# Kernel tuning notes

Measured on AMD Instinct MI355X. Metric: run time of the kernel, lower is better.

## Reference

```python
import jax, jax.numpy as jnp
import numpy as np

DIM = 1024
N_HEADS = 16
HEAD_DIM = DIM // N_HEADS
SCALE = HEAD_DIM ** (-0.5)


def setup_inputs() -> dict:
    key = jax.random.key(0)
    ks = jax.random.split(key, 5)
    B, N = 2, 2048
    x = jax.random.normal(ks[0], (B, N, DIM), dtype=jnp.float32)
    # torch nn.Linear weight layout: (out_features, in_features)
    qkv_w = jax.random.normal(ks[1], (3 * DIM, DIM), dtype=jnp.float32) * 0.02
    qkv_b = jax.random.normal(ks[2], (3 * DIM,), dtype=jnp.float32) * 0.02
    proj_w = jax.random.normal(ks[3], (DIM, DIM), dtype=jnp.float32) * 0.02
    proj_b = jax.random.normal(ks[4], (DIM,), dtype=jnp.float32) * 0.02
    return {"x": x, "qkv_w": qkv_w, "qkv_b": qkv_b, "proj_w": proj_w, "proj_b": proj_b}


def reference(x, qkv_w, qkv_b, proj_w, proj_b):
    B, N, C = x.shape
    # QKV projection: (B,N,C) -> (B,N,3C)
    qkv = jnp.einsum('bnc,oc->bno', x, qkv_w) + qkv_b
    # (B,N,3,H,Dh) -> (3,B,H,N,Dh)
    qkv = qkv.reshape(B, N, 3, N_HEADS, HEAD_DIM).transpose(2, 0, 3, 1, 4)
    q, k, v = qkv[0], qkv[1], qkv[2]
    attn = jnp.einsum('bhqd,bhkd->bhqk', q, k) * SCALE
    attn = jax.nn.softmax(attn, axis=-1)
    out = jnp.einsum('bhqk,bhkd->bhqd', attn, v)
    out = out.transpose(0, 2, 1, 3).reshape(B, N, C)  # concat heads
    out = jnp.einsum('bnc,oc->bno', out, proj_w) + proj_b
    return out
```

## Files before the change

### kernel.cpp

```cpp
#include <hip/hip_runtime.h>

#define DIM 1024
#define NHEADS 16
#define HD 64
#define NSEQ 2048
#define MROWS 4096
#define QKV_LD 3072

typedef __attribute__((ext_vector_type(8))) short short8;
typedef __attribute__((ext_vector_type(4))) short short4v;
typedef __attribute__((ext_vector_type(4))) float f32x4;

typedef __attribute__((address_space(1))) void gvoid_t;
typedef __attribute__((address_space(3))) void lvoid_t;

#if __has_builtin(__builtin_amdgcn_exp2f)
#define EXP2(x) __builtin_amdgcn_exp2f(x)
#else
#define EXP2(x) exp2f(x)
#endif

#if __has_builtin(__builtin_amdgcn_mfma_f32_16x16x16_bf16)
#define MFMA16(a, b, c) __builtin_amdgcn_mfma_f32_16x16x16_bf16(a, b, c, 0, 0, 0)
#elif __has_builtin(__builtin_amdgcn_mfma_f32_16x16x16bf16_1k)
#define MFMA16(a, b, c) __builtin_amdgcn_mfma_f32_16x16x16bf16_1k(a, b, c, 0, 0, 0)
#else
static __device__ __forceinline__ f32x4 mfma16_asm(short4v a, short4v b, f32x4 c) {
  __asm__("v_mfma_f32_16x16x16_bf16 %0, %1, %2, %0" : "+v"(c) : "v"(a), "v"(b));
  return c;
}
#define MFMA16(a, b, c) mfma16_asm(a, b, c)
#endif

#define EXP_SCALE 0.18033688011112042f

__device__ __forceinline__ unsigned short f2bf(float f) {
  unsigned int u = __builtin_bit_cast(unsigned int, f);
  u += 0x7FFFu + ((u >> 16) & 1u);
  return (unsigned short)(u >> 16);
}

__device__ __forceinline__ void gl_lds16(const void* g, void* l) {
  __builtin_amdgcn_global_load_lds((gvoid_t*)g, (lvoid_t*)l, 16, 0, 0);
}

__global__ __launch_bounds__(256) void cast_bf16_3(
    const float* __restrict__ x, const float* __restrict__ wq,
    const float* __restrict__ wp,
    unsigned short* __restrict__ xb, unsigned short* __restrict__ wqb,
    unsigned short* __restrict__ wpb)
{
  int g = blockIdx.x * 256 + threadIdx.x;
  const float* src;
  unsigned short* dst;
  if (g < 1048576)            { src = x  + (size_t)g * 4;              dst = xb  + (size_t)g * 4; }
  else if (g < 1048576 + 786432) { int t = g - 1048576; src = wq + (size_t)t * 4; dst = wqb + (size_t)t * 4; }
  else                        { int t = g - 1048576 - 786432; src = wp + (size_t)t * 4; dst = wpb + (size_t)t * 4; }
  float4 v = *(const float4*)src;
  ushort4 o;
  o.x = f2bf(v.x); o.y = f2bf(v.y); o.z = f2bf(v.z); o.w = f2bf(v.w);
  *(ushort4*)dst = o;
}

__global__ __launch_bounds__(256) void gemm_nt(
    const unsigned short* __restrict__ A,
    const unsigned short* __restrict__ Bw,
    const float* __restrict__ bias,
    int K, int mode,
    unsigned short* __restrict__ oq,
    unsigned short* __restrict__ ovt,
    float* __restrict__ of)
{
  __shared__ unsigned short As[128 * 32];
  __shared__ unsigned short Bs[128 * 32];

  const int tid  = threadIdx.x;
  const int wave = tid >> 6, lane = tid & 63;
  const int quad = lane >> 4, l15 = lane & 15;
  const int mblk = blockIdx.x * 128;
  const int nblk = blockIdx.y * 128;
  const int wrow = (wave >> 1) * 64, wcol = (wave & 1) * 64;

  f32x4 acc[4][4] = {};

  const int sr = lane >> 2;
  const int sq = (lane & 3) ^ (sr & 3);
  const unsigned short* aBase = A  + (size_t)(mblk + wave * 32 + sr) * K + sq * 8;
  const unsigned short* bBase = Bw + (size_t)(nblk + wave * 32 + sr) * K + sq * 8;

  for (int k0 = 0; k0 < K; k0 += 32) {
    __syncthreads();
    gl_lds16(aBase + k0,          As + (wave * 32) * 32);
    gl_lds16(aBase + 16 * K + k0, As + (wave * 32 + 16) * 32);
    gl_lds16(bBase + k0,          Bs + (wave * 32) * 32);
    gl_lds16(bBase + 16 * K + k0, Bs + (wave * 32 + 16) * 32);
    __syncthreads();

    short8 af[4], bf8[4];
#pragma unroll
    for (int mt = 0; mt < 4; ++mt) {
      int row = wrow + mt * 16 + l15;
      af[mt] = *(const short8*)(As + row * 32 + ((quad ^ (row & 3)) * 8));
    }
#pragma unroll
    for (int nt = 0; nt < 4; ++nt) {
      int row = wcol + nt * 16 + l15;
      bf8[nt] = *(const short8*)(Bs + row * 32 + ((quad ^ (row & 3)) * 8));
    }
#pragma unroll
    for (int mt = 0; mt < 4; ++mt)
#pragma unroll
      for (int nt = 0; nt < 4; ++nt)
        acc[mt][nt] = __builtin_amdgcn_mfma_f32_16x16x32_bf16(af[mt], bf8[nt], acc[mt][nt], 0, 0, 0);
  }

  float bv[4];
#pragma unroll
  for (int nt = 0; nt < 4; ++nt) bv[nt] = bias[nblk + wcol + nt * 16 + l15];

  if (mode == 0) {
#pragma unroll
    for (int mt = 0; mt < 4; ++mt) {
      int row0 = mblk + wrow + mt * 16 + quad * 4;
#pragma unroll
      for (int nt = 0; nt < 4; ++nt) {
        int col = nblk + wcol + nt * 16 + l15;
#pragma unroll
        for (int r = 0; r < 4; ++r)
          of[(size_t)(row0 + r) * DIM + col] = acc[mt][nt][r] + bv[nt];
      }
    }
  } else if (nblk < 2048) {
    const float qs = (nblk < 1024) ? EXP_SCALE : 1.0f;
#pragma unroll
    for (int mt = 0; mt < 4; ++mt) {
      int row0 = mblk + wrow + mt * 16 + quad * 4;
#pragma unroll
      for (int nt = 0; nt < 4; ++nt) {
        int col = nblk + wcol + nt * 16 + l15;
#pragma unroll
        for (int r = 0; r < 4; ++r)
          oq[(size_t)(row0 + r) * QKV_LD + col] = f2bf((acc[mt][nt][r] + bv[nt]) * qs);
      }
    }
  } else {
#pragma unroll
    for (int mt = 0; mt < 4; ++mt) {
      int row0 = mblk + wrow + mt * 16 + quad * 4;
      int n0 = row0 & (NSEQ - 1);
      int bb = row0 >> 11;
#pragma unroll
      for (int nt = 0; nt < 4; ++nt) {
        int colr = (nblk - 2048) + wcol + nt * 16 + l15;
        int bh = bb * NHEADS + (colr >> 6);
        int d  = colr & 63;
        ushort4 pk;
        pk.x = f2bf(acc[mt][nt][0] + bv[nt]);
        pk.y = f2bf(acc[mt][nt][1] + bv[nt]);
        pk.z = f2bf(acc[mt][nt][2] + bv[nt]);
        pk.w = f2bf(acc[mt][nt][3] + bv[nt]);
        *(ushort4*)(ovt + ((size_t)bh * HD + d) * NSEQ + n0) = pk;
      }
    }
  }
}

__global__ __launch_bounds__(256) void gemm_nt64(
    const unsigned short* __restrict__ A,
    const unsigned short* __restrict__ Bw,
    const float* __restrict__ bias,
    int K,
    float* __restrict__ of)
{
  __shared__ unsigned short As[64 * 32];
  __shared__ unsigned short Bs[128 * 32];

  const int tid  = threadIdx.x;
  const int wave = tid >> 6, lane = tid & 63;
  const int quad = lane >> 4, l15 = lane & 15;
  const int mblk = blockIdx.x * 64;
  const int nblk = blockIdx.y * 128;
  const int wrow = (wave >> 1) * 32, wcol = (wave & 1) * 64;

  f32x4 acc[2][4] = {};

  const int sr = lane >> 2;
  const int sq = (lane & 3) ^ (sr & 3);
  const unsigned short* aBase = A  + (size_t)(mblk + wave * 16 + sr) * K + sq * 8;
  const unsigned short* bBase = Bw + (size_t)(nblk + wave * 32 + sr) * K + sq * 8;

  for (int k0 = 0; k0 < K; k0 += 32) {
    __syncthreads();
    gl_lds16(aBase + k0,          As + (wave * 16) * 32);
    gl_lds16(bBase + k0,          Bs + (wave * 32) * 32);
    gl_lds16(bBase + 16 * K + k0, Bs + (wave * 32 + 16) * 32);
    __syncthreads();

    short8 af[2], bf8[4];
#pragma unroll
    for (int mt = 0; mt < 2; ++mt) {
      int row = wrow + mt * 16 + l15;
      af[mt] = *(const short8*)(As + row * 32 + ((quad ^ (row & 3)) * 8));
    }
#pragma unroll
    for (int nt = 0; nt < 4; ++nt) {
      int row = wcol + nt * 16 + l15;
      bf8[nt] = *(const short8*)(Bs + row * 32 + ((quad ^ (row & 3)) * 8));
    }
#pragma unroll
    for (int mt = 0; mt < 2; ++mt)
#pragma unroll
      for (int nt = 0; nt < 4; ++nt)
        acc[mt][nt] = __builtin_amdgcn_mfma_f32_16x16x32_bf16(af[mt], bf8[nt], acc[mt][nt], 0, 0, 0);
  }

  float bv[4];
#pragma unroll
  for (int nt = 0; nt < 4; ++nt) bv[nt] = bias[nblk + wcol + nt * 16 + l15];

#pragma unroll
  for (int mt = 0; mt < 2; ++mt) {
    int row0 = mblk + wrow + mt * 16 + quad * 4;
#pragma unroll
    for (int nt = 0; nt < 4; ++nt) {
      int col = nblk + wcol + nt * 16 + l15;
#pragma unroll
      for (int r = 0; r < 4; ++r)
        of[(size_t)(row0 + r) * DIM + col] = acc[mt][nt][r] + bv[nt];
    }
  }
}

__global__ __launch_bounds__(256, 4) void attn_fused(
    const unsigned short* __restrict__ qkv,
    const unsigned short* __restrict__ vt,
    unsigned short* __restrict__ aout)
{
  __shared__ unsigned short Ks[64 * 64];
  __shared__ unsigned short Vs[64 * 64];

  const int tid  = threadIdx.x;
  const int wave = tid >> 6, lane = tid & 63;
  const int quad = lane >> 4, l15 = lane & 15;
  const int bh = blockIdx.x, b = bh >> 4, h = bh & 15;
  const int q0 = blockIdx.y * 64;
  const size_t qkvB = (size_t)b * NSEQ * QKV_LD;

  short8 qf[2];
#pragma unroll
  for (int ks = 0; ks < 2; ++ks)
    qf[ks] = *(const short8*)(qkv + qkvB +
        (size_t)(q0 + wave * 16 + l15) * QKV_LD + h * HD + ks * 32 + quad * 8);

  f32x4 oacc[4] = {};
  float lsum = 0.f;

  const int sr8 = lane >> 3;
  const int sp8 = lane & 7;

  const int r0s = wave * 16 + sr8;
  const int r1s = wave * 16 + 8 + sr8;
  const int qc0 = sp8 ^ (r0s & 7);
  const int qc1 = sp8 ^ (r1s & 7);
  const unsigned short* kBase = qkv + qkvB + DIM + h * HD;
  const unsigned short* vBase = vt + (size_t)bh * HD * NSEQ;
  const unsigned short* kSrc0 = kBase + (size_t)r0s * QKV_LD + qc0 * 8;
  const unsigned short* kSrc1 = kBase + (size_t)r1s * QKV_LD + qc1 * 8;
  const unsigned short* vSrc0 = vBase + (size_t)r0s * NSEQ + qc0 * 8;
  const unsigned short* vSrc1 = vBase + (size_t)r1s * NSEQ + qc1 * 8;

  for (int kk = 0; kk < NSEQ; kk += 64) {
    __syncthreads();
    gl_lds16(kSrc0 + (size_t)kk * QKV_LD, Ks + (wave * 16) * 64);
    gl_lds16(kSrc1 + (size_t)kk * QKV_LD, Ks + (wave * 16 + 8) * 64);
    gl_lds16(vSrc0 + kk,                  Vs + (wave * 16) * 64);
    gl_lds16(vSrc1 + kk,                  Vs + (wave * 16 + 8) * 64);
    __syncthreads();

    short8 kf[4][2];
#pragma unroll
    for (int kt = 0; kt < 4; ++kt)
#pragma unroll
      for (int ks = 0; ks < 2; ++ks) {
        int row = kt * 16 + l15;
        kf[kt][ks] = *(const short8*)(Ks + row * 64 + (((ks * 4 + quad) ^ (row & 7)) * 8));
      }

    f32x4 sacc[4] = {};
    __builtin_amdgcn_s_setprio(1);
#pragma unroll
    for (int kt = 0; kt < 4; ++kt) {
      sacc[kt] = __builtin_amdgcn_mfma_f32_16x16x32_bf16(kf[kt][0], qf[0], sacc[kt], 0, 0, 0);
      sacc[kt] = __builtin_amdgcn_mfma_f32_16x16x32_bf16(kf[kt][1], qf[1], sacc[kt], 0, 0, 0);
    }
    __builtin_amdgcn_s_setprio(0);

    short4v vf[4][4];
#pragma unroll
    for (int dt = 0; dt < 4; ++dt) {
      int row = dt * 16 + l15;
      int rw  = row & 7;
      const unsigned short* vb = Vs + row * 64 + (quad & 1) * 4;
#pragma unroll
      for (int kt = 0; kt < 4; ++kt) {
        int phys = (2 * kt + (quad >> 1)) ^ rw;
        vf[dt][kt] = *(const short4v*)(vb + phys * 8);
      }
    }

#pragma unroll
    for (int kt = 0; kt < 4; ++kt) {
      float p0 = EXP2(sacc[kt][0]);
      float p1 = EXP2(sacc[kt][1]);
      float p2 = EXP2(sacc[kt][2]);
      float p3 = EXP2(sacc[kt][3]);
      lsum += (p0 + p1) + (p2 + p3);
      unsigned r0 = __builtin_bit_cast(unsigned, p0) + 0x8000u;
      unsigned r1 = __builtin_bit_cast(unsigned, p1) + 0x8000u;
      unsigned r2 = __builtin_bit_cast(unsigned, p2) + 0x8000u;
      unsigned r3 = __builtin_bit_cast(unsigned, p3) + 0x8000u;
      uint2 pd;
      pd.x = __builtin_amdgcn_perm(r1, r0, 0x07060302u);
      pd.y = __builtin_amdgcn_perm(r3, r2, 0x07060302u);
      short4v pf = __builtin_bit_cast(short4v, pd);
      __builtin_amdgcn_s_setprio(1);
#pragma unroll
      for (int dt = 0; dt < 4; ++dt)
        oacc[dt] = MFMA16(vf[dt][kt], pf, oacc[dt]);
      __builtin_amdgcn_s_setprio(0);
    }
  }

  lsum += __shfl_xor(lsum, 16);
  lsum += __shfl_xor(lsum, 32);
  float inv = 1.0f / lsum;

  const int qrow = q0 + wave * 16 + l15;
  const size_t outBase = (size_t)(b * NSEQ + qrow) * DIM + h * HD;
#pragma unroll
  for (int dt = 0; dt < 4; ++dt) {
    unsigned a0 = __builtin_bit_cast(unsigned, oacc[dt][0] * inv) + 0x8000u;
    unsigned a1 = __builtin_bit_cast(unsigned, oacc[dt][1] * inv) + 0x8000u;
    unsigned a2 = __builtin_bit_cast(unsigned, oacc[dt][2] * inv) + 0x8000u;
    unsigned a3 = __builtin_bit_cast(unsigned, oacc[dt][3] * inv) + 0x8000u;
    uint2 st;
    st.x = __builtin_amdgcn_perm(a1, a0, 0x07060302u);
    st.y = __builtin_amdgcn_perm(a3, a2, 0x07060302u);
    *(uint2*)(aout + outBase + dt * 16 + quad * 4) = st;
  }
}

extern "C" void kernel_launch(void* const* d_in, const int* in_sizes, int n_in,
                              void* d_out, int out_size, void* d_ws, size_t ws_size,
                              hipStream_t stream) {
  (void)in_sizes; (void)n_in; (void)out_size; (void)ws_size;
  const float* x      = (const float*)d_in[0];
  const float* qkv_w  = (const float*)d_in[1];
  const float* qkv_b  = (const float*)d_in[2];
  const float* proj_w = (const float*)d_in[3];
  const float* proj_b = (const float*)d_in[4];
  float* out = (float*)d_out;

  char* ws = (char*)d_ws;
  unsigned short* xb   = (unsigned short*)(ws);
  unsigned short* wqb  = (unsigned short*)(ws + ( 8u << 20));
  unsigned short* wpb  = (unsigned short*)(ws + (14u << 20));
  unsigned short* qkv  = (unsigned short*)(ws + (16u << 20));
  unsigned short* vtw  = (unsigned short*)(ws + (40u << 20));
  unsigned short* attn = (unsigned short*)(ws + (48u << 20));

  cast_bf16_3<<<8192, 256, 0, stream>>>(x, qkv_w, proj_w, xb, wqb, wpb);
  gemm_nt<<<dim3(32, 24), 256, 0, stream>>>(xb, wqb, qkv_b, DIM, 1, qkv, vtw, nullptr);
  attn_fused<<<dim3(32, 32), 256, 0, stream>>>(qkv, vtw, attn);
  gemm_nt64<<<dim3(64, 8), 256, 0, stream>>>(attn, wpb, proj_b, DIM, out);
}
```

Measured before the change: 192.8 us.

## Double-buffer K/V tiles in attention and store V in MFMA fragment order

The QKV GEMM epilogue now writes V directly in a pre-swizzled fragment layout that matches the per-lane MFMA operand order. The attention kernel can then read V fragments with contiguous 16-byte LDS loads instead of several swizzled 8-byte loads. K/V LDS tiles are double-buffered so the global-to-LDS copy of the next tile overlaps compute on the current tile, leaving one barrier per iteration. LDS use doubles, which may reduce occupancy at 4 blocks per CU, and the V layout is now coupled between the two kernels.

```diff
diff --git a/kernel.cpp b/kernel.cpp
--- a/kernel.cpp
+++ b/kernel.cpp
@@ -149,17 +149,24 @@
       int row0 = mblk + wrow + mt * 16 + quad * 4;
       int n0 = row0 & (NSEQ - 1);
       int bb = row0 >> 11;
+      int tt  = n0 >> 6;
+      int kin = n0 & 63;
+      int kt  = kin >> 4;
+      int qv  = (kin >> 2) & 3;
 #pragma unroll
       for (int nt = 0; nt < 4; ++nt) {
         int colr = (nblk - 2048) + wcol + nt * 16 + l15;
         int bh = bb * NHEADS + (colr >> 6);
         int d  = colr & 63;
+        int dt = d >> 4, dl15 = d & 15;
         ushort4 pk;
         pk.x = f2bf(acc[mt][nt][0] + bv[nt]);
         pk.y = f2bf(acc[mt][nt][1] + bv[nt]);
         pk.z = f2bf(acc[mt][nt][2] + bv[nt]);
         pk.w = f2bf(acc[mt][nt][3] + bv[nt]);
-        *(ushort4*)(ovt + ((size_t)bh * HD + d) * NSEQ + n0) = pk;
+        size_t off = (size_t)(bh * 32 + tt) * 4096 + kt * 1024 + (dt >> 1) * 512
+                   + qv * 128 + dl15 * 8 + (dt & 1) * 4;
+        *(ushort4*)(ovt + off) = pk;
       }
     }
   }
@@ -233,11 +240,11 @@
 
 __global__ __launch_bounds__(256, 4) void attn_fused(
     const unsigned short* __restrict__ qkv,
-    const unsigned short* __restrict__ vt,
+    const unsigned short* __restrict__ vfrag,
     unsigned short* __restrict__ aout)
 {
-  __shared__ unsigned short Ks[64 * 64];
-  __shared__ unsigned short Vs[64 * 64];
+  __shared__ unsigned short Ks[2][64 * 64];
+  __shared__ unsigned short Vs[2][64 * 64];
 
   const int tid  = threadIdx.x;
   const int wave = tid >> 6, lane = tid & 63;
@@ -263,19 +270,28 @@
   const int qc0 = sp8 ^ (r0s & 7);
   const int qc1 = sp8 ^ (r1s & 7);
   const unsigned short* kBase = qkv + qkvB + DIM + h * HD;
-  const unsigned short* vBase = vt + (size_t)bh * HD * NSEQ;
   const unsigned short* kSrc0 = kBase + (size_t)r0s * QKV_LD + qc0 * 8;
   const unsigned short* kSrc1 = kBase + (size_t)r1s * QKV_LD + qc1 * 8;
-  const unsigned short* vSrc0 = vBase + (size_t)r0s * NSEQ + qc0 * 8;
-  const unsigned short* vSrc1 = vBase + (size_t)r1s * NSEQ + qc1 * 8;
+  const unsigned short* vfT = vfrag + (size_t)bh * 32 * 4096 + wave * 512 + lane * 8;
+
+  auto stage = [&](int bufi, int kkn) {
+    gl_lds16(kSrc0 + (size_t)kkn * QKV_LD, &Ks[bufi][(wave * 16) * 64]);
+    gl_lds16(kSrc1 + (size_t)kkn * QKV_LD, &Ks[bufi][(wave * 16 + 8) * 64]);
+    const unsigned short* vs = vfT + (size_t)(kkn >> 6) * 4096;
+    gl_lds16(vs,        &Vs[bufi][wave * 512]);
+    gl_lds16(vs + 2048, &Vs[bufi][wave * 512 + 2048]);
+  };
+
+  stage(0, 0);
+  asm volatile("s_waitcnt vmcnt(0)" ::: "memory");
+  __syncthreads();
 
   for (int kk = 0; kk < NSEQ; kk += 64) {
-    __syncthreads();
-    gl_lds16(kSrc0 + (size_t)kk * QKV_LD, Ks + (wave * 16) * 64);
-    gl_lds16(kSrc1 + (size_t)kk * QKV_LD, Ks + (wave * 16 + 8) * 64);
-    gl_lds16(vSrc0 + kk,                  Vs + (wave * 16) * 64);
-    gl_lds16(vSrc1 + kk,                  Vs + (wave * 16 + 8) * 64);
-    __syncthreads();
+    const int cur = (kk >> 6) & 1;
+    if (kk + 64 < NSEQ) stage(cur ^ 1, kk + 64);
+
+    const unsigned short* Kc = Ks[cur];
+    const unsigned short* Vc = Vs[cur];
 
     short8 kf[4][2];
 #pragma unroll
@@ -283,7 +299,7 @@
 #pragma unroll
       for (int ks = 0; ks < 2; ++ks) {
         int row = kt * 16 + l15;
-        kf[kt][ks] = *(const short8*)(Ks + row * 64 + (((ks * 4 + quad) ^ (row & 7)) * 8));
+        kf[kt][ks] = *(const short8*)(Kc + row * 64 + (((ks * 4 + quad) ^ (row & 7)) * 8));
       }
 
     f32x4 sacc[4] = {};
@@ -297,16 +313,13 @@
 
     short4v vf[4][4];
 #pragma unroll
-    for (int dt = 0; dt < 4; ++dt) {
-      int row = dt * 16 + l15;
-      int rw  = row & 7;
-      const unsigned short* vb = Vs + row * 64 + (quad & 1) * 4;
-#pragma unroll
-      for (int kt = 0; kt < 4; ++kt) {
-        int phys = (2 * kt + (quad >> 1)) ^ rw;
-        vf[dt][kt] = *(const short4v*)(vb + phys * 8);
-      }
-    }
+    for (int kt = 0; kt < 4; ++kt)
+#pragma unroll
+      for (int p = 0; p < 2; ++p) {
+        short8 vv = *(const short8*)(Vc + kt * 1024 + p * 512 + lane * 8);
+        vf[2 * p    ][kt] = __builtin_shufflevector(vv, vv, 0, 1, 2, 3);
+        vf[2 * p + 1][kt] = __builtin_shufflevector(vv, vv, 4, 5, 6, 7);
+      }
 
 #pragma unroll
     for (int kt = 0; kt < 4; ++kt) {
@@ -329,6 +342,9 @@
         oacc[dt] = MFMA16(vf[dt][kt], pf, oacc[dt]);
       __builtin_amdgcn_s_setprio(0);
     }
+
+    asm volatile("s_waitcnt vmcnt(0)" ::: "memory");
+    __syncthreads();
   }
 
   lsum += __shfl_xor(lsum, 16);
```

After: 190.8 us. Within noise of the previous version (-1.0%).
